# Performance work log

Measured on AMD Instinct MI355X. Metric: run time of the kernel, lower is better.

The kernel has to match this reference:

```python
import jax, jax.numpy as jnp
import numpy as np

N = 4096     # num nodes
FEAT = 500   # knn attribute dim
HID = 512    # args.hid_dim
E = 65536    # edges (avg degree 16)
T = 8        # args.time -> euler steps with step_size=1


def setup_inputs() -> dict:
    key = jax.random.key(0)
    ks = jax.random.split(key, 10)
    knn = jax.random.normal(ks[0], (N, FEAT), jnp.float32)
    adj = jax.random.uniform(ks[1], (N, N), jnp.float32)
    norm_factor = jnp.ones((), jnp.float32)
    edge_index = jax.random.randint(ks[2], (2, E), 0, N, dtype=jnp.int32).astype(jnp.int64)
    edge_weight = jax.random.uniform(ks[3], (E,), jnp.float32)
    # AGCN params (init eye + small noise so math is non-trivial)
    w1 = jnp.eye(N, dtype=jnp.float32) + 0.01 * jax.random.normal(ks[4], (N, N), jnp.float32)
    w2 = jnp.eye(N, dtype=jnp.float32) + 0.01 * jax.random.normal(ks[5], (N, N), jnp.float32)
    # extractor: Linear(N, HID) then Linear(HID, HID), kaiming-normal (relu), zero bias
    W0 = jax.random.normal(ks[6], (HID, N), jnp.float32) * np.float32((2.0 / N) ** 0.5)
    b0 = jnp.zeros((HID,), jnp.float32)
    W1 = jax.random.normal(ks[7], (HID, HID), jnp.float32) * np.float32((2.0 / HID) ** 0.5)
    b1 = jnp.zeros((HID,), jnp.float32)
    # LaplacianODEFunc scalar params
    alpha_train = jnp.asarray(0.5, jnp.float32)
    beta_train = jnp.asarray(0.1, jnp.float32)
    return dict(knn=knn, adj=adj, norm_factor=norm_factor, w1=w1, w2=w2,
                W0=W0, b0=b0, W1=W1, b1=b1, edge_weight=edge_weight,
                alpha_train=alpha_train, beta_train=beta_train, edge_index=edge_index)


def _spmm(edge_index, edge_weight, x):
    # out[row] += w * x[col], row=edge_index[0], col=edge_index[1]
    msg = edge_weight[:, None] * x[edge_index[1]]          # [E, HID]
    return jax.ops.segment_sum(msg, edge_index[0], num_segments=x.shape[0])


def reference(knn, adj, norm_factor, w1, w2, W0, b0, W1, b1,
              edge_weight, alpha_train, beta_train, edge_index):
    # ---- AGCN ----
    H = (adj @ w1) @ adj.T                                  # [N, N]
    H = (H @ w2) @ knn                                      # [N, FEAT]
    embed = H @ H.T                                         # [N, N]
    norm = jnp.maximum(jnp.linalg.norm(embed, axis=1, keepdims=True), 1e-12)
    embed = embed / norm                                    # F.normalize(dim=1)
    # ---- extractor MLP (no activation in source; dropout=eval no-op) ----
    h = embed @ W0.T + b0                                   # [N, HID]
    h = h @ W1.T + b1                                       # [N, HID]
    # ---- ODE diffusion: dx/dt = sigmoid(a)*(Ax - x) + b*x0, explicit Euler dt=1 ----
    x0 = jax.lax.stop_gradient(h)
    alpha = jax.nn.sigmoid(alpha_train)

    def step(x, _):
        ax = _spmm(edge_index, edge_weight, x)
        return x + alpha * (ax - x) + beta_train * x0, None

    z_ode, _ = jax.lax.scan(step, h, None, length=T)
    z = jax.nn.relu(norm_factor * z_ode + h)
    z = (z - z.mean(0)) / jnp.std(z, ddof=1)                # torch std is unbiased
    return z
```

## Files before the change

kernel.cpp:

```cpp
#include <hip/hip_runtime.h>
#include <stdint.h>
#include <stddef.h>

typedef __bf16 bf16;
typedef __attribute__((ext_vector_type(8))) __bf16 bf16x8;
typedef __attribute__((ext_vector_type(4))) __bf16 bf16x4;
typedef __attribute__((ext_vector_type(4))) float f32x4;

#define NN 4096
#define HIDD 512
#define NE 65536

__device__ inline void gll16(const void* g, void* l) {
    __builtin_amdgcn_global_load_lds(
        (const __attribute__((address_space(1))) void*)g,
        (__attribute__((address_space(3))) void*)l, 16, 0, 0);
}

__global__ void cvt_f32_bf16(const float* __restrict__ in, bf16* __restrict__ out, int n) {
    int i = (blockIdx.x * 256 + threadIdx.x) * 4;
    if (i >= n) return;
    float4 v = *reinterpret_cast<const float4*>(in + i);
    bf16x4 o;
    o[0] = (bf16)v.x; o[1] = (bf16)v.y; o[2] = (bf16)v.z; o[3] = (bf16)v.w;
    *reinterpret_cast<bf16x4*>(out + i) = o;
}

__global__ void reduce_bf16_slices(const bf16* __restrict__ in, bf16* __restrict__ out,
                                   int n, int S) {
    int i = (blockIdx.x * 256 + threadIdx.x) * 8;
    if (i >= n) return;
    float acc[8] = {};
    for (int k = 0; k < S; ++k) {
        bf16x8 v = *reinterpret_cast<const bf16x8*>(in + (size_t)k * n + i);
#pragma unroll
        for (int j = 0; j < 8; ++j) acc[j] += (float)v[j];
    }
    bf16x8 o;
#pragma unroll
    for (int j = 0; j < 8; ++j) o[j] = (bf16)acc[j];
    *reinterpret_cast<bf16x8*>(out + i) = o;
}

__global__ void transpose_pad_f32(const float* __restrict__ in, bf16* __restrict__ out,
                                  int R, int C, int Cpad) {
    __shared__ bf16 tile[32][33];
    int c0 = blockIdx.x * 32, r0 = blockIdx.y * 32;
    int tx = threadIdx.x, ty = threadIdx.y;
    for (int i = ty; i < 32; i += 8) {
        int r = r0 + i, c = c0 + tx;
        bf16 v = (bf16)0.f;
        if (r < R && c < C) v = (bf16)in[(size_t)r * C + c];
        tile[i][tx] = v;
    }
    __syncthreads();
    for (int i = ty; i < 32; i += 8) {
        int oc = c0 + i, orow = r0 + tx;
        if (oc < Cpad && orow < R) out[(size_t)oc * R + orow] = tile[tx][i];
    }
}

__global__ void transpose_dual_f32(const float* __restrict__ in, bf16* __restrict__ outT,
                                   bf16* __restrict__ outD, int Nn) {
    __shared__ bf16 tile[64][66];
    int r0 = blockIdx.y * 64, c0 = blockIdx.x * 64;
    int t = threadIdx.x;
    int tx = t & 7;
    int ty = t >> 3;
#pragma unroll
    for (int i = 0; i < 2; ++i) {
        int r = ty + i * 32;
        const float* src = in + (size_t)(r0 + r) * Nn + c0 + tx * 8;
        float4 v0 = *reinterpret_cast<const float4*>(src);
        float4 v1 = *reinterpret_cast<const float4*>(src + 4);
        bf16x8 o;
        o[0] = (bf16)v0.x; o[1] = (bf16)v0.y; o[2] = (bf16)v0.z; o[3] = (bf16)v0.w;
        o[4] = (bf16)v1.x; o[5] = (bf16)v1.y; o[6] = (bf16)v1.z; o[7] = (bf16)v1.w;
        *reinterpret_cast<bf16x8*>(&tile[r][tx * 8]) = o;
        *reinterpret_cast<bf16x8*>(outD + (size_t)(r0 + r) * Nn + c0 + tx * 8) = o;
    }
    __syncthreads();
    int c = t >> 2;
    int rsb = (t & 3) * 16;
#pragma unroll
    for (int j = 0; j < 2; ++j) {
        int r = rsb + j * 8;
        bf16x8 o;
#pragma unroll
        for (int e = 0; e < 8; ++e) o[e] = tile[r + e][c];
        *reinterpret_cast<bf16x8*>(outT + (size_t)(c0 + c) * Nn + r0 + r) = o;
    }
}

__global__ void transpose_bf16(const bf16* __restrict__ in, bf16* __restrict__ out,
                               int R, int C) {
    __shared__ bf16 tile[32][33];
    int c0 = blockIdx.x * 32, r0 = blockIdx.y * 32;
    int tx = threadIdx.x, ty = threadIdx.y;
    for (int i = ty; i < 32; i += 8)
        tile[i][tx] = in[(size_t)(r0 + i) * C + c0 + tx];
    __syncthreads();
    for (int i = ty; i < 32; i += 8)
        out[(size_t)(c0 + i) * R + r0 + tx] = tile[tx][i];
}

template<int OMODE, bool HAS_BIAS, bool ROW_SCALE>
__global__ __launch_bounds__(256)
void gemm_nt(const bf16* __restrict__ A, const bf16* __restrict__ B,
             void* __restrict__ Cp, const float* __restrict__ bias,
             const float* __restrict__ rowscale, int M, int N, int K) {
    __shared__ __align__(16) bf16 As[3][128 * 32];
    __shared__ __align__(16) bf16 Bs[3][128 * 32];
    const int tid  = threadIdx.x;
    const int wave = tid >> 6;
    const int lane = tid & 63;
    const int m0 = blockIdx.y * 128, n0 = blockIdx.x * 128;
    const int lrow = lane >> 2;
    const int lcol = ((lane & 3) ^ ((lane >> 3) & 3)) * 8;
    const int c0 = wave * 2;
    const size_t arow0 = (size_t)(m0 + c0 * 16 + lrow) * K + lcol;
    const size_t arow1 = (size_t)(m0 + (c0 + 1) * 16 + lrow) * K + lcol;
    const size_t brow0 = (size_t)(n0 + c0 * 16 + lrow) * K + lcol;
    const size_t brow1 = (size_t)(n0 + (c0 + 1) * 16 + lrow) * K + lcol;

    f32x4 acc[4][4] = {};

    const int wm = (wave >> 1) * 64;
    const int wn = (wave & 1) * 64;
    const int fm = wm + (lane & 15);
    const int fn = wn + (lane & 15);
    const int fk = ((lane >> 4) ^ ((lane >> 1) & 3)) * 8;

    const int kper = K / gridDim.z;
    const int kz0 = blockIdx.z * kper;
    const int nt = kper >> 5;

    auto stage = [&](int t, int buf) {
        const int k0 = kz0 + (t << 5);
        gll16(A + arow0 + k0, &As[buf][c0 * 512]);
        gll16(A + arow1 + k0, &As[buf][(c0 + 1) * 512]);
        gll16(B + brow0 + k0, &Bs[buf][c0 * 512]);
        gll16(B + brow1 + k0, &Bs[buf][(c0 + 1) * 512]);
    };

    stage(0, 0);
    if (nt > 1) stage(1, 1);

    int cur = 0;
    for (int t = 0; t < nt; ++t) {
        if (t + 1 < nt) asm volatile("s_waitcnt vmcnt(4)" ::: "memory");
        else            asm volatile("s_waitcnt vmcnt(0)" ::: "memory");
        __builtin_amdgcn_s_barrier();
        if (t + 2 < nt) {
            int nb = cur + 2; if (nb >= 3) nb -= 3;
            stage(t + 2, nb);
        }
        bf16x8 af[4], bg[4];
#pragma unroll
        for (int i = 0; i < 4; ++i)
            af[i] = *reinterpret_cast<const bf16x8*>(&As[cur][(fm + i * 16) * 32 + fk]);
#pragma unroll
        for (int j = 0; j < 4; ++j)
            bg[j] = *reinterpret_cast<const bf16x8*>(&Bs[cur][(fn + j * 16) * 32 + fk]);
#pragma unroll
        for (int i = 0; i < 4; ++i)
#pragma unroll
            for (int j = 0; j < 4; ++j)
                acc[i][j] = __builtin_amdgcn_mfma_f32_16x16x32_bf16(af[i], bg[j], acc[i][j], 0, 0, 0);
        cur = (cur + 1 == 3) ? 0 : cur + 1;
    }

    const int rbase = m0 + wm + (lane >> 4) * 4;
    const int cbase = n0 + wn + (lane & 15);
    float* outf = (float*)Cp + (size_t)blockIdx.z * M * N;
    bf16*  outb = (bf16*)Cp;
    bf16*  outp = (bf16*)Cp + (size_t)blockIdx.z * M * N;
#pragma unroll
    for (int i = 0; i < 4; ++i) {
#pragma unroll
        for (int j = 0; j < 4; ++j) {
            int col = cbase + j * 16;
            float bv = 0.f;
            if (HAS_BIAS) bv = bias[col];
#pragma unroll
            for (int r = 0; r < 4; ++r) {
                int row = rbase + i * 16 + r;
                float v = acc[i][j][r];
                if (ROW_SCALE) v *= rowscale[row];
                v += bv;
                if (OMODE == 0)      outf[(size_t)row * N + col] = v;
                else if (OMODE == 1) outb[(size_t)row * N + col] = (bf16)v;
                else                 outp[(size_t)row * N + col] = (bf16)v;
            }
        }
    }
}

__global__ void colnorm_part(const bf16* __restrict__ Ht, const float* __restrict__ Rf,
                             float* __restrict__ n2) {
    int i = blockIdx.x * 128 + threadIdx.x;
    int a0 = blockIdx.y * 64;
    const float* Rf2 = Rf + (size_t)HIDD * NN;
    float s = 0.f;
    for (int a = a0; a < a0 + 64; ++a) {
        size_t idx = (size_t)a * NN + i;
        s += (Rf[idx] + Rf2[idx]) * (float)Ht[idx];
    }
    atomicAdd(&n2[i], s);
}

__global__ void colnorm_fin(const float* __restrict__ n2, float* __restrict__ inv) {
    int i = blockIdx.x * 256 + threadIdx.x;
    inv[i] = 1.f / fmaxf(sqrtf(n2[i]), 1e-12f);
}

__global__ void bias_fuse(const float* __restrict__ W1, const float* __restrict__ b0,
                          const float* __restrict__ b1, float* __restrict__ bp) {
    int row = blockIdx.x * 4 + (threadIdx.x >> 6);
    int lane = threadIdx.x & 63;
    const float4* wr = (const float4*)(W1 + (size_t)row * HIDD);
    const float4* bz = (const float4*)b0;
    float s = 0.f;
#pragma unroll
    for (int j = 0; j < 2; ++j) {
        float4 a = wr[lane * 2 + j], b = bz[lane * 2 + j];
        s += a.x * b.x + a.y * b.y + a.z * b.z + a.w * b.w;
    }
    for (int off = 32; off; off >>= 1) s += __shfl_down(s, off);
    if (lane == 0) bp[row] = b1[row] + s;
}

__global__ void reduce2_scale_bias(const bf16* __restrict__ p, bf16* __restrict__ out,
                                   const float* __restrict__ inv, const float* __restrict__ bp) {
    int i = (blockIdx.x * 256 + threadIdx.x) * 8;
    const int n = NN * HIDD;
    bf16x8 a = *reinterpret_cast<const bf16x8*>(p + i);
    bf16x8 b = *reinterpret_cast<const bf16x8*>(p + n + i);
    int row = i >> 9;
    int col = i & (HIDD - 1);
    float sc = inv[row];
    bf16x8 o;
#pragma unroll
    for (int j = 0; j < 8; ++j)
        o[j] = (bf16)(((float)a[j] + (float)b[j]) * sc + bp[col + j]);
    *reinterpret_cast<bf16x8*>(out + i) = o;
}

__global__ void csr_count(const int* __restrict__ ei, int* __restrict__ cnt, int E) {
    int e = blockIdx.x * 256 + threadIdx.x;
    if (e < E) atomicAdd(&cnt[ei[e]], 1);
}

__global__ void scan_4096(const int* __restrict__ cnt, int* __restrict__ rs) {
    __shared__ int s[1024];
    int t = threadIdx.x;
    int b = t * 4;
    int a0 = cnt[b], a1 = cnt[b + 1], a2 = cnt[b + 2], a3 = cnt[b + 3];
    int tot = a0 + a1 + a2 + a3;
    s[t] = tot;
    __syncthreads();
    for (int off = 1; off < 1024; off <<= 1) {
        int v = (t >= off) ? s[t - off] : 0;
        __syncthreads();
        s[t] += v;
        __syncthreads();
    }
    int excl = s[t] - tot;
    rs[b] = excl; rs[b + 1] = excl + a0; rs[b + 2] = excl + a0 + a1; rs[b + 3] = excl + a0 + a1 + a2;
    if (t == 1023) rs[4096] = s[1023];
}

__global__ void csr_scatter(const int* __restrict__ ei, const float* __restrict__ ew,
                            int* __restrict__ cur, int* __restrict__ ccol,
                            float* __restrict__ cw, int E) {
    int e = blockIdx.x * 256 + threadIdx.x;
    if (e < E) {
        int r = ei[e];
        int p = atomicAdd(&cur[r], 1);
        ccol[p] = ei[E + e];
        cw[p] = ew[e];
    }
}

__global__ void ode_step_bf16(const bf16* __restrict__ xin, const bf16* __restrict__ x0,
                              bf16* __restrict__ xout, const int* __restrict__ rs,
                              const int* __restrict__ ccol, const float* __restrict__ cw,
                              const float* __restrict__ alpha_p, const float* __restrict__ beta_p) {
    int row = blockIdx.x * 4 + (threadIdx.x >> 6);
    int lane = threadIdx.x & 63;
    float alpha = 1.f / (1.f + expf(-alpha_p[0]));
    float beta = beta_p[0];
    const bf16x8* xin8 = (const bf16x8*)xin;
    float acc[8] = {};
    int p0 = rs[row], p1 = rs[row + 1];
    for (int p = p0; p < p1; ++p) {
        int c = ccol[p]; float w = cw[p];
        bf16x8 v = xin8[(size_t)c * 64 + lane];
#pragma unroll
        for (int j = 0; j < 8; ++j) acc[j] += w * (float)v[j];
    }
    bf16x8 xi = xin8[(size_t)row * 64 + lane];
    bf16x8 xz = ((const bf16x8*)x0)[(size_t)row * 64 + lane];
    bf16x8 r;
#pragma unroll
    for (int j = 0; j < 8; ++j) {
        float x = (float)xi[j];
        r[j] = (bf16)(x + alpha * (acc[j] - x) + beta * (float)xz[j]);
    }
    ((bf16x8*)xout)[(size_t)row * 64 + lane] = r;
}

__global__ void epi1(const bf16* __restrict__ x8, const bf16* __restrict__ h,
                     const float* __restrict__ nf_p, float* __restrict__ z,
                     float* __restrict__ colsum, float* __restrict__ gst) {
    __shared__ float r1[512], r2[512];
    int b = blockIdx.x, j = threadIdx.x;
    float nf = nf_p[0];
    float cp = 0.f, sq = 0.f;
    for (int i = 0; i < 8; ++i) {
        size_t idx = (size_t)(b * 8 + i) * HIDD + j;
        float v = nf * (float)x8[idx] + (float)h[idx];
        v = fmaxf(v, 0.f);
        z[idx] = v;
        cp += v; sq += v * v;
    }
    atomicAdd(&colsum[j], cp);
    r1[j] = cp; r2[j] = sq;
    __syncthreads();
    for (int off = 256; off > 0; off >>= 1) {
        if (j < off) { r1[j] += r1[j + off]; r2[j] += r2[j + off]; }
        __syncthreads();
    }
    if (j == 0) { atomicAdd(&gst[0], r1[0]); atomicAdd(&gst[1], r2[0]); }
}

__global__ void epi2(const float* __restrict__ z, const float* __restrict__ colsum,
                     const float* __restrict__ gst, float* __restrict__ out) {
    size_t idx = (size_t)blockIdx.x * 256 + threadIdx.x;
    int j = (int)(idx & (HIDD - 1));
    float n = (float)NN * (float)HIDD;
    float gmean = gst[0] / n;
    float var = (gst[1] - n * gmean * gmean) / (n - 1.f);
    float istd = rsqrtf(var);
    float mean = colsum[j] * (1.f / (float)NN);
    out[idx] = (z[idx] - mean) * istd;
}

extern "C" void kernel_launch(void* const* d_in, const int* in_sizes, int n_in,
                              void* d_out, int out_size, void* d_ws, size_t ws_size,
                              hipStream_t stream) {
    const float* knn  = (const float*)d_in[0];
    const float* adj  = (const float*)d_in[1];
    const float* nf   = (const float*)d_in[2];
    const float* w1   = (const float*)d_in[3];
    const float* w2   = (const float*)d_in[4];
    const float* W0   = (const float*)d_in[5];
    const float* b0   = (const float*)d_in[6];
    const float* W1   = (const float*)d_in[7];
    const float* b1   = (const float*)d_in[8];
    const float* ew   = (const float*)d_in[9];
    const float* alph = (const float*)d_in[10];
    const float* beta = (const float*)d_in[11];
    const int*   ei   = (const int*)d_in[12];

    char* w = (char*)d_ws;
    size_t off = 0;
    auto alloc = [&](size_t bytes) -> char* {
        char* p = w + off;
        off += (bytes + 255) & ~(size_t)255;
        return p;
    };
    const size_t SZ_NN  = (size_t)NN * NN * sizeof(bf16);
    const size_t SZ_TH  = (size_t)HIDD * NN * sizeof(bf16);
    bf16* Bar  = (bf16*)alloc(SZ_NN);
    bf16* Car  = (bf16*)alloc(SZ_NN);
    bf16* Adjb = (bf16*)alloc(SZ_NN);
    bf16* knnT = (bf16*)alloc(SZ_TH);
    bf16* tA   = (bf16*)alloc(SZ_TH);
    bf16* tB   = (bf16*)alloc(SZ_TH);
    float* tf  = (float*)alloc((size_t)32 * 1024 * 1024);
    bf16* Hm   = (bf16*)alloc(SZ_TH);
    bf16* Gb   = (bf16*)alloc((size_t)HIDD * HIDD * sizeof(bf16));
    bf16* M0b  = (bf16*)alloc((size_t)HIDD * HIDD * sizeof(bf16));
    bf16* Qtb  = (bf16*)alloc((size_t)HIDD * HIDD * sizeof(bf16));
    bf16* hb   = (bf16*)alloc((size_t)NN * HIDD * sizeof(bf16));
    float* inv = (float*)alloc(NN * sizeof(float));
    float* n2  = (float*)alloc(NN * sizeof(float));
    int*  cnt  = (int*)alloc(NN * sizeof(int));
    int*  rs   = (int*)alloc((NN + 1) * sizeof(int));
    int*  cur  = (int*)alloc(NN * sizeof(int));
    int*  ccol = (int*)alloc(NE * sizeof(int));
    float* cw  = (float*)alloc(NE * sizeof(float));
    float* colsum = (float*)alloc(HIDD * sizeof(float));
    float* gst = (float*)alloc(2 * sizeof(float));
    float* bp  = (float*)alloc(HIDD * sizeof(float));
    bf16* tfb = (bf16*)tf;
    bf16* W1b = (bf16*)((char*)Car + 16 * 1024 * 1024);
    bf16* xA  = (bf16*)Car;
    bf16* xB  = (bf16*)Car + (size_t)NN * HIDD;
    (void)ws_size; (void)n_in; (void)in_sizes; (void)out_size;

    dim3 tb(32, 8);
    const int nTH = HIDD * NN;
    const int nHH = HIDD * HIDD;

    transpose_pad_f32<<<dim3(16, 128), tb, 0, stream>>>(knn, knnT, NN, 500, HIDD);
    cvt_f32_bf16<<<(NN * NN) / 1024, 256, 0, stream>>>(w2, Car, NN * NN);
    transpose_dual_f32<<<dim3(64, 64), 256, 0, stream>>>(adj, Bar, Adjb, NN);

    gemm_nt<2, false, false><<<dim3(32, 4, 4), 256, 0, stream>>>(knnT, Car, tfb, nullptr, nullptr, HIDD, NN, NN);
    reduce_bf16_slices<<<nTH / 2048, 256, 0, stream>>>(tfb, tA, nTH, 4);
    gemm_nt<2, false, false><<<dim3(32, 4, 4), 256, 0, stream>>>(tA, Bar, tfb, nullptr, nullptr, HIDD, NN, NN);
    reduce_bf16_slices<<<nTH / 2048, 256, 0, stream>>>(tfb, tB, nTH, 4);
    cvt_f32_bf16<<<(NN * NN) / 1024, 256, 0, stream>>>(w1, Car, NN * NN);
    gemm_nt<2, false, false><<<dim3(32, 4, 4), 256, 0, stream>>>(tB, Car, tfb, nullptr, nullptr, HIDD, NN, NN);
    reduce_bf16_slices<<<nTH / 2048, 256, 0, stream>>>(tfb, tA, nTH, 4);
    gemm_nt<2, false, false><<<dim3(32, 4, 4), 256, 0, stream>>>(tA, Adjb, tfb, nullptr, nullptr, HIDD, NN, NN);
    reduce_bf16_slices<<<nTH / 2048, 256, 0, stream>>>(tfb, tB, nTH, 4);

    transpose_bf16<<<dim3(128, 16), tb, 0, stream>>>(tB, Hm, HIDD, NN);

    gemm_nt<2, false, false><<<dim3(4, 4, 32), 256, 0, stream>>>(tB, tB, tfb, nullptr, nullptr, HIDD, HIDD, NN);
    reduce_bf16_slices<<<nHH / 2048, 256, 0, stream>>>(tfb, Gb, nHH, 32);

    gemm_nt<0, false, false><<<dim3(32, 4, 2), 256, 0, stream>>>(Gb, Hm, tf, nullptr, nullptr, HIDD, NN, HIDD);
    hipMemsetAsync(n2, 0, NN * sizeof(float), stream);
    colnorm_part<<<dim3(32, 8), 128, 0, stream>>>(tB, tf, n2);
    colnorm_fin<<<NN / 256, 256, 0, stream>>>(n2, inv);

    cvt_f32_bf16<<<(HIDD * NN) / 1024, 256, 0, stream>>>(W0, Car, HIDD * NN);
    gemm_nt<2, false, false><<<dim3(4, 4, 32), 256, 0, stream>>>(tB, Car, tfb, nullptr, nullptr, HIDD, HIDD, NN);
    reduce_bf16_slices<<<nHH / 2048, 256, 0, stream>>>(tfb, M0b, nHH, 32);

    cvt_f32_bf16<<<(HIDD * HIDD) / 1024, 256, 0, stream>>>(W1, W1b, HIDD * HIDD);
    gemm_nt<2, false, false><<<dim3(4, 4, 8), 256, 0, stream>>>(W1b, M0b, tfb, nullptr, nullptr, HIDD, HIDD, HIDD);
    reduce_bf16_slices<<<nHH / 2048, 256, 0, stream>>>(tfb, Qtb, nHH, 8);

    bias_fuse<<<128, 256, 0, stream>>>(W1, b0, b1, bp);

    gemm_nt<2, false, false><<<dim3(4, 32, 2), 256, 0, stream>>>(Hm, Qtb, tfb, nullptr, nullptr, NN, HIDD, HIDD);
    reduce2_scale_bias<<<(NN * HIDD) / 2048, 256, 0, stream>>>(tfb, hb, inv, bp);

    hipMemsetAsync(cnt, 0, NN * sizeof(int), stream);
    csr_count<<<NE / 256, 256, 0, stream>>>(ei, cnt, NE);
    scan_4096<<<1, 1024, 0, stream>>>(cnt, rs);
    hipMemcpyAsync(cur, rs, NN * sizeof(int), hipMemcpyDeviceToDevice, stream);
    csr_scatter<<<NE / 256, 256, 0, stream>>>(ei, ew, cur, ccol, cw, NE);

    const bf16* xi = hb;
    bf16* xo = xA;
    for (int s = 0; s < 8; ++s) {
        ode_step_bf16<<<NN / 4, 256, 0, stream>>>(xi, hb, xo, rs, ccol, cw, alph, beta);
        xi = xo;
        xo = (s % 2 == 0) ? xB : xA;
    }

    hipMemsetAsync(colsum, 0, HIDD * sizeof(float), stream);
    hipMemsetAsync(gst, 0, 2 * sizeof(float), stream);
    epi1<<<NN / 8, 512, 0, stream>>>(xB, hb, nf, tf, colsum, gst);
    epi2<<<(NN * HIDD) / 256, 256, 0, stream>>>(tf, colsum, gst, (float*)d_out);
}
```

Before: 645.2 us.

## Enlarge GEMM tiles to 256x128, batch weight conversions, fuse small epilogue kernels

The GEMM block tile grows to 256x128 with 8x4 accumulators per wave and launch bounds of 2 blocks per CU, and split-K factors are doubled so the grid size stays similar. All weight fp32-to-bf16 conversions move into one up-front kernel with separate buffers. Several small kernels are also merged: colnorm_fin folds into the reduce/scale kernel, a memcpy folds into the scan, and epi2 recomputes z from bf16 instead of reading an fp32 intermediate. The aim is better data reuse in the GEMMs, fewer launches, and less traffic, at the cost of more registers, more LDS, and larger split-K partial buffers.

```diff
diff --git a/kernel.cpp b/kernel.cpp
--- a/kernel.cpp
+++ b/kernel.cpp
@@ -17,13 +17,23 @@
         (__attribute__((address_space(3))) void*)l, 16, 0, 0);
 }
 
-__global__ void cvt_f32_bf16(const float* __restrict__ in, bf16* __restrict__ out, int n) {
+__global__ void cvt_all(const float* __restrict__ w2, bf16* __restrict__ o2,
+                        const float* __restrict__ w1, bf16* __restrict__ o1,
+                        const float* __restrict__ W0, bf16* __restrict__ oW0,
+                        const float* __restrict__ W1, bf16* __restrict__ oW1) {
+    const int NW = NN * NN;
+    const int T1 = 2 * NW;
+    const int T2 = T1 + HIDD * NN;
     int i = (blockIdx.x * 256 + threadIdx.x) * 4;
-    if (i >= n) return;
-    float4 v = *reinterpret_cast<const float4*>(in + i);
+    const float* src; bf16* dst; int k;
+    if (i < NW)       { src = w2; dst = o2;  k = i; }
+    else if (i < T1)  { src = w1; dst = o1;  k = i - NW; }
+    else if (i < T2)  { src = W0; dst = oW0; k = i - T1; }
+    else              { src = W1; dst = oW1; k = i - T2; }
+    float4 v = *reinterpret_cast<const float4*>(src + k);
     bf16x4 o;
     o[0] = (bf16)v.x; o[1] = (bf16)v.y; o[2] = (bf16)v.z; o[3] = (bf16)v.w;
-    *reinterpret_cast<bf16x4*>(out + i) = o;
+    *reinterpret_cast<bf16x4*>(dst + k) = o;
 }
 
 __global__ void reduce_bf16_slices(const bf16* __restrict__ in, bf16* __restrict__ out,
@@ -65,31 +75,31 @@
     __shared__ bf16 tile[64][66];
     int r0 = blockIdx.y * 64, c0 = blockIdx.x * 64;
     int t = threadIdx.x;
-    int tx = t & 7;
-    int ty = t >> 3;
+    int cg = t & 7, rr = t >> 3;
 #pragma unroll
     for (int i = 0; i < 2; ++i) {
-        int r = ty + i * 32;
-        const float* src = in + (size_t)(r0 + r) * Nn + c0 + tx * 8;
+        int r = rr + i * 32;
+        const float* src = in + (size_t)(r0 + r) * Nn + c0 + cg * 8;
         float4 v0 = *reinterpret_cast<const float4*>(src);
         float4 v1 = *reinterpret_cast<const float4*>(src + 4);
-        bf16x8 o;
-        o[0] = (bf16)v0.x; o[1] = (bf16)v0.y; o[2] = (bf16)v0.z; o[3] = (bf16)v0.w;
-        o[4] = (bf16)v1.x; o[5] = (bf16)v1.y; o[6] = (bf16)v1.z; o[7] = (bf16)v1.w;
-        *reinterpret_cast<bf16x8*>(&tile[r][tx * 8]) = o;
-        *reinterpret_cast<bf16x8*>(outD + (size_t)(r0 + r) * Nn + c0 + tx * 8) = o;
+        union { bf16x8 b; unsigned int u[4]; } cv;
+        cv.b[0] = (bf16)v0.x; cv.b[1] = (bf16)v0.y; cv.b[2] = (bf16)v0.z; cv.b[3] = (bf16)v0.w;
+        cv.b[4] = (bf16)v1.x; cv.b[5] = (bf16)v1.y; cv.b[6] = (bf16)v1.z; cv.b[7] = (bf16)v1.w;
+        *reinterpret_cast<bf16x8*>(outD + (size_t)(r0 + r) * Nn + c0 + cg * 8) = cv.b;
+        unsigned int* tw = reinterpret_cast<unsigned int*>(&tile[r][cg * 8]);
+#pragma unroll
+        for (int k = 0; k < 4; ++k) tw[k] = cv.u[k];
     }
     __syncthreads();
-    int c = t >> 2;
-    int rsb = (t & 3) * 16;
-#pragma unroll
-    for (int j = 0; j < 2; ++j) {
-        int r = rsb + j * 8;
-        bf16x8 o;
-#pragma unroll
-        for (int e = 0; e < 8; ++e) o[e] = tile[r + e][c];
-        *reinterpret_cast<bf16x8*>(outT + (size_t)(c0 + c) * Nn + r0 + r) = o;
-    }
+    int oc = t >> 3, rseg = (t & 7) * 8;
+    bf16x8 w0, w1;
+#pragma unroll
+    for (int e = 0; e < 8; ++e) {
+        w0[e] = tile[rseg + e][oc];
+        w1[e] = tile[rseg + e][oc + 32];
+    }
+    *reinterpret_cast<bf16x8*>(outT + (size_t)(c0 + oc) * Nn + r0 + rseg) = w0;
+    *reinterpret_cast<bf16x8*>(outT + (size_t)(c0 + oc + 32) * Nn + r0 + rseg) = w1;
 }
 
 __global__ void transpose_bf16(const bf16* __restrict__ in, bf16* __restrict__ out,
@@ -105,27 +115,30 @@
 }
 
 template<int OMODE, bool HAS_BIAS, bool ROW_SCALE>
-__global__ __launch_bounds__(256)
+__global__ __launch_bounds__(256, 2)
 void gemm_nt(const bf16* __restrict__ A, const bf16* __restrict__ B,
              void* __restrict__ Cp, const float* __restrict__ bias,
              const float* __restrict__ rowscale, int M, int N, int K) {
-    __shared__ __align__(16) bf16 As[3][128 * 32];
+    __shared__ __align__(16) bf16 As[3][256 * 32];
     __shared__ __align__(16) bf16 Bs[3][128 * 32];
     const int tid  = threadIdx.x;
     const int wave = tid >> 6;
     const int lane = tid & 63;
-    const int m0 = blockIdx.y * 128, n0 = blockIdx.x * 128;
+    const int m0 = blockIdx.y * 256, n0 = blockIdx.x * 128;
     const int lrow = lane >> 2;
     const int lcol = ((lane & 3) ^ ((lane >> 3) & 3)) * 8;
-    const int c0 = wave * 2;
-    const size_t arow0 = (size_t)(m0 + c0 * 16 + lrow) * K + lcol;
-    const size_t arow1 = (size_t)(m0 + (c0 + 1) * 16 + lrow) * K + lcol;
-    const size_t brow0 = (size_t)(n0 + c0 * 16 + lrow) * K + lcol;
-    const size_t brow1 = (size_t)(n0 + (c0 + 1) * 16 + lrow) * K + lcol;
-
-    f32x4 acc[4][4] = {};
-
-    const int wm = (wave >> 1) * 64;
+    const int ca = wave * 4;
+    const int cb = wave * 2;
+    size_t arow[4];
+#pragma unroll
+    for (int q = 0; q < 4; ++q)
+        arow[q] = (size_t)(m0 + (ca + q) * 16 + lrow) * K + lcol;
+    const size_t brow0 = (size_t)(n0 + cb * 16 + lrow) * K + lcol;
+    const size_t brow1 = (size_t)(n0 + (cb + 1) * 16 + lrow) * K + lcol;
+
+    f32x4 acc[8][4] = {};
+
+    const int wm = (wave >> 1) * 128;
     const int wn = (wave & 1) * 64;
     const int fm = wm + (lane & 15);
     const int fn = wn + (lane & 15);
@@ -137,10 +150,11 @@
 
     auto stage = [&](int t, int buf) {
         const int k0 = kz0 + (t << 5);
-        gll16(A + arow0 + k0, &As[buf][c0 * 512]);
-        gll16(A + arow1 + k0, &As[buf][(c0 + 1) * 512]);
-        gll16(B + brow0 + k0, &Bs[buf][c0 * 512]);
-        gll16(B + brow1 + k0, &Bs[buf][(c0 + 1) * 512]);
+#pragma unroll
+        for (int q = 0; q < 4; ++q)
+            gll16(A + arow[q] + k0, &As[buf][(ca + q) * 512]);
+        gll16(B + brow0 + k0, &Bs[buf][cb * 512]);
+        gll16(B + brow1 + k0, &Bs[buf][(cb + 1) * 512]);
     };
 
     stage(0, 0);
@@ -148,22 +162,22 @@
 
     int cur = 0;
     for (int t = 0; t < nt; ++t) {
-        if (t + 1 < nt) asm volatile("s_waitcnt vmcnt(4)" ::: "memory");
+        if (t + 1 < nt) asm volatile("s_waitcnt vmcnt(6)" ::: "memory");
         else            asm volatile("s_waitcnt vmcnt(0)" ::: "memory");
         __builtin_amdgcn_s_barrier();
         if (t + 2 < nt) {
             int nb = cur + 2; if (nb >= 3) nb -= 3;
             stage(t + 2, nb);
         }
-        bf16x8 af[4], bg[4];
-#pragma unroll
-        for (int i = 0; i < 4; ++i)
+        bf16x8 af[8], bg[4];
+#pragma unroll
+        for (int i = 0; i < 8; ++i)
             af[i] = *reinterpret_cast<const bf16x8*>(&As[cur][(fm + i * 16) * 32 + fk]);
 #pragma unroll
         for (int j = 0; j < 4; ++j)
             bg[j] = *reinterpret_cast<const bf16x8*>(&Bs[cur][(fn + j * 16) * 32 + fk]);
 #pragma unroll
-        for (int i = 0; i < 4; ++i)
+        for (int i = 0; i < 8; ++i)
 #pragma unroll
             for (int j = 0; j < 4; ++j)
                 acc[i][j] = __builtin_amdgcn_mfma_f32_16x16x32_bf16(af[i], bg[j], acc[i][j], 0, 0, 0);
@@ -176,7 +190,7 @@
     bf16*  outb = (bf16*)Cp;
     bf16*  outp = (bf16*)Cp + (size_t)blockIdx.z * M * N;
 #pragma unroll
-    for (int i = 0; i < 4; ++i) {
+    for (int i = 0; i < 8; ++i) {
 #pragma unroll
         for (int j = 0; j < 4; ++j) {
             int col = cbase + j * 16;
@@ -200,18 +214,14 @@
                              float* __restrict__ n2) {
     int i = blockIdx.x * 128 + threadIdx.x;
     int a0 = blockIdx.y * 64;
-    const float* Rf2 = Rf + (size_t)HIDD * NN;
+    const size_t n = (size_t)HIDD * NN;
     float s = 0.f;
     for (int a = a0; a < a0 + 64; ++a) {
         size_t idx = (size_t)a * NN + i;
-        s += (Rf[idx] + Rf2[idx]) * (float)Ht[idx];
+        float r = Rf[idx] + Rf[n + idx] + Rf[2 * n + idx] + Rf[3 * n + idx];
+        s += r * (float)Ht[idx];
     }
     atomicAdd(&n2[i], s);
-}
-
-__global__ void colnorm_fin(const float* __restrict__ n2, float* __restrict__ inv) {
-    int i = blockIdx.x * 256 + threadIdx.x;
-    inv[i] = 1.f / fmaxf(sqrtf(n2[i]), 1e-12f);
 }
 
 __global__ void bias_fuse(const float* __restrict__ W1, const float* __restrict__ b0,
@@ -230,19 +240,24 @@
     if (lane == 0) bp[row] = b1[row] + s;
 }
 
-__global__ void reduce2_scale_bias(const bf16* __restrict__ p, bf16* __restrict__ out,
-                                   const float* __restrict__ inv, const float* __restrict__ bp) {
+__global__ void reduce4_scale_bias(const bf16* __restrict__ p, bf16* __restrict__ out,
+                                   const float* __restrict__ n2, const float* __restrict__ bp) {
     int i = (blockIdx.x * 256 + threadIdx.x) * 8;
     const int n = NN * HIDD;
-    bf16x8 a = *reinterpret_cast<const bf16x8*>(p + i);
-    bf16x8 b = *reinterpret_cast<const bf16x8*>(p + n + i);
+    float acc[8] = {};
+#pragma unroll
+    for (int s = 0; s < 4; ++s) {
+        bf16x8 v = *reinterpret_cast<const bf16x8*>(p + (size_t)s * n + i);
+#pragma unroll
+        for (int j = 0; j < 8; ++j) acc[j] += (float)v[j];
+    }
     int row = i >> 9;
     int col = i & (HIDD - 1);
-    float sc = inv[row];
+    float sc = 1.f / fmaxf(sqrtf(n2[row]), 1e-12f);
     bf16x8 o;
 #pragma unroll
     for (int j = 0; j < 8; ++j)
-        o[j] = (bf16)(((float)a[j] + (float)b[j]) * sc + bp[col + j]);
+        o[j] = (bf16)(acc[j] * sc + bp[col + j]);
     *reinterpret_cast<bf16x8*>(out + i) = o;
 }
 
@@ -251,7 +266,8 @@
     if (e < E) atomicAdd(&cnt[ei[e]], 1);
 }
 
-__global__ void scan_4096(const int* __restrict__ cnt, int* __restrict__ rs) {
+__global__ void scan_4096(const int* __restrict__ cnt, int* __restrict__ rs,
+                          int* __restrict__ cur) {
     __shared__ int s[1024];
     int t = threadIdx.x;
     int b = t * 4;
@@ -267,6 +283,7 @@
     }
     int excl = s[t] - tot;
     rs[b] = excl; rs[b + 1] = excl + a0; rs[b + 2] = excl + a0 + a1; rs[b + 3] = excl + a0 + a1 + a2;
+    cur[b] = excl; cur[b + 1] = excl + a0; cur[b + 2] = excl + a0 + a1; cur[b + 3] = excl + a0 + a1 + a2;
     if (t == 1023) rs[4096] = s[1023];
 }
 
@@ -311,7 +328,7 @@
 }
 
 __global__ void epi1(const bf16* __restrict__ x8, const bf16* __restrict__ h,
-                     const float* __restrict__ nf_p, float* __restrict__ z,
+                     const float* __restrict__ nf_p,
                      float* __restrict__ colsum, float* __restrict__ gst) {
     __shared__ float r1[512], r2[512];
     int b = blockIdx.x, j = threadIdx.x;
@@ -321,7 +338,6 @@
         size_t idx = (size_t)(b * 8 + i) * HIDD + j;
         float v = nf * (float)x8[idx] + (float)h[idx];
         v = fmaxf(v, 0.f);
-        z[idx] = v;
         cp += v; sq += v * v;
     }
     atomicAdd(&colsum[j], cp);
@@ -334,16 +350,30 @@
     if (j == 0) { atomicAdd(&gst[0], r1[0]); atomicAdd(&gst[1], r2[0]); }
 }
 
-__global__ void epi2(const float* __restrict__ z, const float* __restrict__ colsum,
+__global__ void epi2(const bf16* __restrict__ x8, const bf16* __restrict__ h,
+                     const float* __restrict__ nf_p, const float* __restrict__ colsum,
                      const float* __restrict__ gst, float* __restrict__ out) {
-    size_t idx = (size_t)blockIdx.x * 256 + threadIdx.x;
-    int j = (int)(idx & (HIDD - 1));
+    int i = (blockIdx.x * 256 + threadIdx.x) * 8;
+    float nf = nf_p[0];
     float n = (float)NN * (float)HIDD;
     float gmean = gst[0] / n;
     float var = (gst[1] - n * gmean * gmean) / (n - 1.f);
     float istd = rsqrtf(var);
-    float mean = colsum[j] * (1.f / (float)NN);
-    out[idx] = (z[idx] - mean) * istd;
+    int col = i & (HIDD - 1);
+    bf16x8 xv = *reinterpret_cast<const bf16x8*>(x8 + i);
+    bf16x8 hv = *reinterpret_cast<const bf16x8*>(h + i);
+    float4 o0, o1;
+    float ov[8];
+#pragma unroll
+    for (int j = 0; j < 8; ++j) {
+        float v = fmaxf(nf * (float)xv[j] + (float)hv[j], 0.f);
+        float mean = colsum[col + j] * (1.f / (float)NN);
+        ov[j] = (v - mean) * istd;
+    }
+    o0.x = ov[0]; o0.y = ov[1]; o0.z = ov[2]; o0.w = ov[3];
+    o1.x = ov[4]; o1.y = ov[5]; o1.z = ov[6]; o1.w = ov[7];
+    *reinterpret_cast<float4*>(out + i) = o0;
+    *reinterpret_cast<float4*>(out + i + 4) = o1;
 }
 
 extern "C" void kernel_launch(void* const* d_in, const int* in_sizes, int n_in,
@@ -375,16 +405,18 @@
     bf16* Bar  = (bf16*)alloc(SZ_NN);
     bf16* Car  = (bf16*)alloc(SZ_NN);
     bf16* Adjb = (bf16*)alloc(SZ_NN);
+    bf16* W1big= (bf16*)alloc(SZ_NN);
     bf16* knnT = (bf16*)alloc(SZ_TH);
     bf16* tA   = (bf16*)alloc(SZ_TH);
     bf16* tB   = (bf16*)alloc(SZ_TH);
     float* tf  = (float*)alloc((size_t)32 * 1024 * 1024);
     bf16* Hm   = (bf16*)alloc(SZ_TH);
+    bf16* W0b  = (bf16*)alloc(SZ_TH);
+    bf16* W1sb = (bf16*)alloc((size_t)HIDD * HIDD * sizeof(bf16));
     bf16* Gb   = (bf16*)alloc((size_t)HIDD * HIDD * sizeof(bf16));
     bf16* M0b  = (bf16*)alloc((size_t)HIDD * HIDD * sizeof(bf16));
     bf16* Qtb  = (bf16*)alloc((size_t)HIDD * HIDD * sizeof(bf16));
     bf16* hb   = (bf16*)alloc((size_t)NN * HIDD * sizeof(bf16));
-    float* inv = (float*)alloc(NN * sizeof(float));
     float* n2  = (float*)alloc(NN * sizeof(float));
     int*  cnt  = (int*)alloc(NN * sizeof(int));
     int*  rs   = (int*)alloc((NN + 1) * sizeof(int));
@@ -395,7 +427,6 @@
     float* gst = (float*)alloc(2 * sizeof(float));
     float* bp  = (float*)alloc(HIDD * sizeof(float));
     bf16* tfb = (bf16*)tf;
-    bf16* W1b = (bf16*)((char*)Car + 16 * 1024 * 1024);
     bf16* xA  = (bf16*)Car;
     bf16* xB  = (bf16*)Car + (size_t)NN * HIDD;
     (void)ws_size; (void)n_in; (void)in_sizes; (void)out_size;
@@ -404,47 +435,42 @@
     const int nTH = HIDD * NN;
     const int nHH = HIDD * HIDD;
 
+    cvt_all<<<35072, 256, 0, stream>>>(w2, Car, w1, W1big, W0, W0b, W1, W1sb);
     transpose_pad_f32<<<dim3(16, 128), tb, 0, stream>>>(knn, knnT, NN, 500, HIDD);
-    cvt_f32_bf16<<<(NN * NN) / 1024, 256, 0, stream>>>(w2, Car, NN * NN);
     transpose_dual_f32<<<dim3(64, 64), 256, 0, stream>>>(adj, Bar, Adjb, NN);
 
-    gemm_nt<2, false, false><<<dim3(32, 4, 4), 256, 0, stream>>>(knnT, Car, tfb, nullptr, nullptr, HIDD, NN, NN);
-    reduce_bf16_slices<<<nTH / 2048, 256, 0, stream>>>(tfb, tA, nTH, 4);
-    gemm_nt<2, false, false><<<dim3(32, 4, 4), 256, 0, stream>>>(tA, Bar, tfb, nullptr, nullptr, HIDD, NN, NN);
-    reduce_bf16_slices<<<nTH / 2048, 256, 0, stream>>>(tfb, tB, nTH, 4);
-    cvt_f32_bf16<<<(NN * NN) / 1024, 256, 0, stream>>>(w1, Car, NN * NN);
-    gemm_nt<2, false, false><<<dim3(32, 4, 4), 256, 0, stream>>>(tB, Car, tfb, nullptr, nullptr, HIDD, NN, NN);
-    reduce_bf16_slices<<<nTH / 2048, 256, 0, stream>>>(tfb, tA, nTH, 4);
-    gemm_nt<2, false, false><<<dim3(32, 4, 4), 256, 0, stream>>>(tA, Adjb, tfb, nullptr, nullptr, HIDD, NN, NN);
-    reduce_bf16_slices<<<nTH / 2048, 256, 0, stream>>>(tfb, tB, nTH, 4);
+    gemm_nt<2, false, false><<<dim3(32, 2, 8), 256, 0, stream>>>(knnT, Car, tfb, nullptr, nullptr, HIDD, NN, NN);
+    reduce_bf16_slices<<<nTH / 2048, 256, 0, stream>>>(tfb, tA, nTH, 8);
+    gemm_nt<2, false, false><<<dim3(32, 2, 8), 256, 0, stream>>>(tA, Bar, tfb, nullptr, nullptr, HIDD, NN, NN);
+    reduce_bf16_slices<<<nTH / 2048, 256, 0, stream>>>(tfb, tB, nTH, 8);
+    gemm_nt<2, false, false><<<dim3(32, 2, 8), 256, 0, stream>>>(tB, W1big, tfb, nullptr, nullptr, HIDD, NN, NN);
+    reduce_bf16_slices<<<nTH / 2048, 256, 0, stream>>>(tfb, tA, nTH, 8);
+    gemm_nt<2, false, false><<<dim3(32, 2, 8), 256, 0, stream>>>(tA, Adjb, tfb, nullptr, nullptr, HIDD, NN, NN);
+    reduce_bf16_slices<<<nTH / 2048, 256, 0, stream>>>(tfb, tB, nTH, 8);
 
     transpose_bf16<<<dim3(128, 16), tb, 0, stream>>>(tB, Hm, HIDD, NN);
 
-    gemm_nt<2, false, false><<<dim3(4, 4, 32), 256, 0, stream>>>(tB, tB, tfb, nullptr, nullptr, HIDD, HIDD, NN);
+    gemm_nt<2, false, false><<<dim3(4, 2, 32), 256, 0, stream>>>(tB, tB, tfb, nullptr, nullptr, HIDD, HIDD, NN);
     reduce_bf16_slices<<<nHH / 2048, 256, 0, stream>>>(tfb, Gb, nHH, 32);
 
-    gemm_nt<0, false, false><<<dim3(32, 4, 2), 256, 0, stream>>>(Gb, Hm, tf, nullptr, nullptr, HIDD, NN, HIDD);
+    gemm_nt<0, false, false><<<dim3(32, 2, 4), 256, 0, stream>>>(Gb, Hm, tf, nullptr, nullptr, HIDD, NN, HIDD);
     hipMemsetAsync(n2, 0, NN * sizeof(float), stream);
     colnorm_part<<<dim3(32, 8), 128, 0, stream>>>(tB, tf, n2);
-    colnorm_fin<<<NN / 256, 256, 0, stream>>>(n2, inv);
-
-    cvt_f32_bf16<<<(HIDD * NN) / 1024, 256, 0, stream>>>(W0, Car, HIDD * NN);
-    gemm_nt<2, false, false><<<dim3(4, 4, 32), 256, 0, stream>>>(tB, Car, tfb, nullptr, nullptr, HIDD, HIDD, NN);
+
+    gemm_nt<2, false, false><<<dim3(4, 2, 32), 256, 0, stream>>>(tB, W0b, tfb, nullptr, nullptr, HIDD, HIDD, NN);
     reduce_bf16_slices<<<nHH / 2048, 256, 0, stream>>>(tfb, M0b, nHH, 32);
 
-    cvt_f32_bf16<<<(HIDD * HIDD) / 1024, 256, 0, stream>>>(W1, W1b, HIDD * HIDD);
-    gemm_nt<2, false, false><<<dim3(4, 4, 8), 256, 0, stream>>>(W1b, M0b, tfb, nullptr, nullptr, HIDD, HIDD, HIDD);
+    gemm_nt<2, false, false><<<dim3(4, 2, 8), 256, 0, stream>>>(W1sb, M0b, tfb, nullptr, nullptr, HIDD, HIDD, HIDD);
     reduce_bf16_slices<<<nHH / 2048, 256, 0, stream>>>(tfb, Qtb, nHH, 8);
 
     bias_fuse<<<128, 256, 0, stream>>>(W1, b0, b1, bp);
 
-    gemm_nt<2, false, false><<<dim3(4, 32, 2), 256, 0, stream>>>(Hm, Qtb, tfb, nullptr, nullptr, NN, HIDD, HIDD);
-    reduce2_scale_bias<<<(NN * HIDD) / 2048, 256, 0, stream>>>(tfb, hb, inv, bp);
+    gemm_nt<2, false, false><<<dim3(4, 16, 4), 256, 0, stream>>>(Hm, Qtb, tfb, nullptr, nullptr, NN, HIDD, HIDD);
+    reduce4_scale_bias<<<(NN * HIDD) / 2048, 256, 0, stream>>>(tfb, hb, n2, bp);
 
     hipMemsetAsync(cnt, 0, NN * sizeof(int), stream);
     csr_count<<<NE / 256, 256, 0, stream>>>(ei, cnt, NE);
-    scan_4096<<<1, 1024, 0, stream>>>(cnt, rs);
-    hipMemcpyAsync(cur, rs, NN * sizeof(int), hipMemcpyDeviceToDevice, stream);
+    scan_4096<<<1, 1024, 0, stream>>>(cnt, rs, cur);
     csr_scatter<<<NE / 256, 256, 0, stream>>>(ei, ew, cur, ccol, cw, NE);
 
     const bf16* xi = hb;
@@ -457,6 +483,6 @@
 
     hipMemsetAsync(colsum, 0, HIDD * sizeof(float), stream);
     hipMemsetAsync(gst, 0, 2 * sizeof(float), stream);
-    epi1<<<NN / 8, 512, 0, stream>>>(xB, hb, nf, tf, colsum, gst);
-    epi2<<<(NN * HIDD) / 256, 256, 0, stream>>>(tf, colsum, gst, (float*)d_out);
-}
+    epi1<<<NN / 8, 512, 0, stream>>>(xB, hb, nf, colsum, gst);
+    epi2<<<(NN * HIDD) / 2048, 256, 0, stream>>>(xB, hb, nf, colsum, gst, (float*)d_out);
+}
```

New measurement: 650.4 us. No clear change (+0.8%).
